# Kernel optimization log

Hardware: AMD Instinct MI355X
Metric: run time of the kernel (lower is better)

The kernel has to match this reference:

```python
import jax, jax.numpy as jnp
import numpy as np

N = 50000      # nodes
E = 800000     # edges (before self-loops)
H = 4          # heads
C = 64         # hidden channels per head
CLS = 10       # len(bins)+1
D_IN = 64      # input feature dim
NEG_SLOPE = 0.2


def setup_inputs() -> dict:
    key = jax.random.key(0)
    ks = jax.random.split(key, 24)
    inp = {
        "x": jax.random.normal(ks[0], (N, D_IN), jnp.float32),
        "edge_index": jax.random.randint(ks[1], (2, E), 0, N),
    }
    dims = [(D_IN, C), (H * C, C), (H * C, C), (H * C, C), (H * C, CLS)]
    k = 2
    for l, (din, dout) in enumerate(dims):
        sc = 1.0 / np.sqrt(din)
        inp[f"W{l}"] = jax.random.normal(ks[k], (din, H * dout), jnp.float32) * sc; k += 1
        inp[f"as{l}"] = jax.random.normal(ks[k], (H, dout), jnp.float32) * sc; k += 1
        inp[f"ad{l}"] = jax.random.normal(ks[k], (H, dout), jnp.float32) * sc; k += 1
        inp[f"b{l}"] = jnp.zeros((H * dout,), jnp.float32)
    return inp


def gat_layer(x, src, dst, W, a_s, a_d, b):
    # PyG GATConv (concat=True): h = x W -> [N,H,Ch]
    Hh, Ch = a_s.shape
    h = (x @ W).reshape(-1, Hh, Ch)
    asn = (h * a_s).sum(-1)                      # [N,H]
    adn = (h * a_d).sum(-1)                      # [N,H]
    e = jax.nn.leaky_relu(asn[src] + adn[dst], NEG_SLOPE)   # [Et,H]
    m = jax.ops.segment_max(e, dst, num_segments=N)         # softmax over in-edges per dst
    ex = jnp.exp(e - m[dst])
    s = jax.ops.segment_sum(ex, dst, num_segments=N)
    alpha = ex / (s[dst] + 1e-16)                # [Et,H]
    out = jax.ops.segment_sum(alpha[:, :, None] * h[src], dst, num_segments=N)
    return out.reshape(-1, Hh * Ch) + b


def reference(x, edge_index, W0, as0, ad0, b0, W1, as1, ad1, b1,
              W2, as2, ad2, b2, W3, as3, ad3, b3, W4, as4, ad4, b4):
    loop = jnp.arange(N, dtype=edge_index.dtype)  # GATConv add_self_loops=True
    src = jnp.concatenate([edge_index[0], loop])
    dst = jnp.concatenate([edge_index[1], loop])
    params = [(W0, as0, ad0, b0), (W1, as1, ad1, b1), (W2, as2, ad2, b2),
              (W3, as3, ad3, b3), (W4, as4, ad4, b4)]
    for W, a_s, a_d, b in params:
        x = jax.nn.relu(gat_layer(x, src, dst, W, a_s, a_d, b))
        # dropout(p=0.5) is identity in eval mode (training=False)
    return x
```

## Files before the change

### kernel.cpp

```cpp
#include <hip/hip_runtime.h>
#include <hip/hip_bf16.h>
#include <math.h>

#define N_NODES 50000
#define N_PAD   50048
#define N_EDGES 800000
#define HEADS 4

typedef __attribute__((ext_vector_type(8))) _Float16 half8_t;
typedef __attribute__((ext_vector_type(4))) float f32x4;

__device__ inline void split2(float v, _Float16& p0, _Float16& p1) {
    p0 = (_Float16)v;
    p1 = (_Float16)(v - (float)p0);
}


__global__ void init_deg_kernel(int* __restrict__ deg) {
    int i = blockIdx.x * blockDim.x + threadIdx.x;
    if (i < N_NODES) deg[i] = 1;
}

__global__ void hist_kernel(const int* __restrict__ dst, int* __restrict__ deg) {
    int i = blockIdx.x * blockDim.x + threadIdx.x;
    if (i < N_EDGES) atomicAdd(&deg[dst[i]], 1);
}

__global__ __launch_bounds__(1024) void scan_kernel(const int* __restrict__ deg,
                                                    int* __restrict__ rowptr,
                                                    int* __restrict__ cursor) {
    __shared__ int wsums[16];
    const int t = threadIdx.x;
    const int wv = t >> 6, ln = t & 63;
    const int WCHUNK = (N_NODES + 15) / 16;
    const int base = wv * WCHUNK;
    int lim = base + WCHUNK; if (lim > N_NODES) lim = N_NODES;

    int tot = 0;
    for (int i = base + ln; i < lim; i += 64) tot += deg[i];
#pragma unroll
    for (int o = 1; o < 64; o <<= 1) tot += __shfl_xor(tot, o);
    if (ln == 0) wsums[wv] = tot;
    __syncthreads();

    int run = 0;
    for (int w = 0; w < wv; ++w) run += wsums[w];

    for (int i0 = base; i0 < lim; i0 += 64) {
        int i = i0 + ln;
        int d = (i < lim) ? deg[i] : 0;
        int sc = d;
#pragma unroll
        for (int o = 1; o < 64; o <<= 1) {
            int v = __shfl_up(sc, o);
            if (ln >= o) sc += v;
        }
        if (i < lim) {
            int val = run + sc - d;
            rowptr[i] = val;
            cursor[i] = val;
        }
        run += __shfl(sc, 63);
    }
    if (t == 1023) rowptr[N_NODES] = run;
}

__global__ void scatter_kernel(const int* __restrict__ src, const int* __restrict__ dst,
                               int* __restrict__ cursor, int* __restrict__ col) {
    int i = blockIdx.x * blockDim.x + threadIdx.x;
    if (i < N_EDGES) {
        int d = dst[i];
        int pos = atomicAdd(&cursor[d], 1);
        col[pos] = src[i];
    } else if (i < N_EDGES + N_NODES) {
        int n = i - N_EDGES;
        int pos = atomicAdd(&cursor[n], 1);
        col[pos] = n;
    }
}


__global__ void x_split_kernel(const float* __restrict__ x, _Float16* __restrict__ pl,
                               size_t pstride) {
    int i = blockIdx.x * blockDim.x + threadIdx.x;
    if (i >= N_NODES * 64) return;
    _Float16 a, b;
    split2(x[i], a, b);
    pl[i] = a;
    pl[pstride + i] = b;
}

__global__ void w_split_kernel(const float* __restrict__ W, _Float16* __restrict__ wt,
                               int K, int NC) {
    int t = blockIdx.x * blockDim.x + threadIdx.x;
    int c = t >> 8, k = t & 255;
    float v = (k < K && c < NC) ? W[k * NC + c] : 0.f;
    _Float16 a, b;
    split2(v, a, b);
    wt[t] = a;
    wt[65536 + t] = b;
}


template <int FUSE_ATTN>
__global__ __launch_bounds__(256) void gemm_mfma_kernel(
        const _Float16* __restrict__ Apl, size_t apstride, int lda,
        const _Float16* __restrict__ Wt,
        float* __restrict__ C, int K, int NC,
        const float* __restrict__ as_flat, const float* __restrict__ ad_flat,
        float* __restrict__ asn, float* __restrict__ adn) {
    __shared__ _Float16 As[2][128][40];
    __shared__ _Float16 Bs[2][128][40];

    const int tid = threadIdx.x;
    const int lane = tid & 63;
    const int wave = tid >> 6;
    const int wr = (wave >> 1) * 64;
    const int wc = (wave & 1) * 64;
    const int m0 = blockIdx.x * 128;
    const int n0 = blockIdx.y * 128;

    f32x4 acc[4][4];
#pragma unroll
    for (int i = 0; i < 4; ++i)
#pragma unroll
        for (int j = 0; j < 4; ++j) acc[i][j] = (f32x4){0.f, 0.f, 0.f, 0.f};

    const int row0 = tid >> 2, q = tid & 3;
    const int row1 = row0 + 64;

    const _Float16* aptr0 = Apl + (size_t)(m0 + row0) * lda + q * 8;
    const _Float16* aptr1 = Apl + (size_t)(m0 + row1) * lda + q * 8;
    const _Float16* bptr0 = Wt + (size_t)(n0 + row0) * 256 + q * 8;
    const _Float16* bptr1 = Wt + (size_t)(n0 + row1) * 256 + q * 8;

    half8_t pa[2][2], pb[2][2];
#pragma unroll
    for (int p = 0; p < 2; ++p) {
        pa[p][0] = *(const half8_t*)(aptr0 + p * apstride);
        pa[p][1] = *(const half8_t*)(aptr1 + p * apstride);
        pb[p][0] = *(const half8_t*)(bptr0 + p * 65536);
        pb[p][1] = *(const half8_t*)(bptr1 + p * 65536);
    }

    for (int k0 = 0; k0 < K; k0 += 32) {
        if (k0) __syncthreads();
#pragma unroll
        for (int p = 0; p < 2; ++p) {
            *(half8_t*)(&As[p][row0][q * 8]) = pa[p][0];
            *(half8_t*)(&As[p][row1][q * 8]) = pa[p][1];
            *(half8_t*)(&Bs[p][row0][q * 8]) = pb[p][0];
            *(half8_t*)(&Bs[p][row1][q * 8]) = pb[p][1];
        }
        __syncthreads();

        if (k0 + 32 < K) {
            int kn = k0 + 32;
#pragma unroll
            for (int p = 0; p < 2; ++p) {
                pa[p][0] = *(const half8_t*)(aptr0 + p * apstride + kn);
                pa[p][1] = *(const half8_t*)(aptr1 + p * apstride + kn);
                pb[p][0] = *(const half8_t*)(bptr0 + p * 65536 + kn);
                pb[p][1] = *(const half8_t*)(bptr1 + p * 65536 + kn);
            }
        }

        half8_t bf[2][4];
#pragma unroll
        for (int p = 0; p < 2; ++p)
#pragma unroll
            for (int j = 0; j < 4; ++j)
                bf[p][j] = *(const half8_t*)(&Bs[p][wc + j * 16 + (lane & 15)][(lane >> 4) * 8]);

#pragma unroll
        for (int i = 0; i < 4; ++i) {
            half8_t af0 = *(const half8_t*)(&As[0][wr + i * 16 + (lane & 15)][(lane >> 4) * 8]);
            half8_t af1 = *(const half8_t*)(&As[1][wr + i * 16 + (lane & 15)][(lane >> 4) * 8]);
#pragma unroll
            for (int j = 0; j < 4; ++j) {
                f32x4 c = acc[i][j];
                c = __builtin_amdgcn_mfma_f32_16x16x32_f16(af0, bf[1][j], c, 0, 0, 0);
                c = __builtin_amdgcn_mfma_f32_16x16x32_f16(af1, bf[0][j], c, 0, 0, 0);
                c = __builtin_amdgcn_mfma_f32_16x16x32_f16(af0, bf[0][j], c, 0, 0, 0);
                acc[i][j] = c;
            }
        }
    }

    const int rbase = m0 + wr + (lane >> 4) * 4;
    const int cbase = n0 + wc + (lane & 15);
#pragma unroll
    for (int i = 0; i < 4; ++i)
#pragma unroll
        for (int j = 0; j < 4; ++j) {
            int gcol = cbase + j * 16;
            if (gcol >= NC) continue;
#pragma unroll
            for (int r4 = 0; r4 < 4; ++r4) {
                int grow = rbase + i * 16 + r4;
                if (grow < N_NODES) C[(size_t)grow * NC + gcol] = acc[i][j][r4];
            }
        }

    if (FUSE_ATTN) {
        const int hd_out = (n0 + wc) >> 6;
        float as_v[4], ad_v[4];
#pragma unroll
        for (int j = 0; j < 4; ++j) {
            int gc = cbase + j * 16;
            as_v[j] = as_flat[gc];
            ad_v[j] = ad_flat[gc];
        }
#pragma unroll
        for (int i = 0; i < 4; ++i)
#pragma unroll
            for (int r4 = 0; r4 < 4; ++r4) {
                float ps = 0.f, pd = 0.f;
#pragma unroll
                for (int j = 0; j < 4; ++j) {
                    float v = acc[i][j][r4];
                    ps += v * as_v[j];
                    pd += v * ad_v[j];
                }
#pragma unroll
                for (int o = 1; o < 16; o <<= 1) {
                    ps += __shfl_xor(ps, o);
                    pd += __shfl_xor(pd, o);
                }
                if ((lane & 15) == 0) {
                    int grow = rbase + i * 16 + r4;
                    if (grow < N_NODES) {
                        asn[grow * 4 + hd_out] = ps;
                        adn[grow * 4 + hd_out] = pd;
                    }
                }
            }
    }
}


__global__ void attn_coef_kernel(const float* __restrict__ h,
                                 const float* __restrict__ a_s,
                                 const float* __restrict__ a_d,
                                 float* __restrict__ asn, float* __restrict__ adn,
                                 int CH) {
    int t = blockIdx.x * blockDim.x + threadIdx.x;
    if (t >= N_NODES * HEADS) return;
    int n = t >> 2;
    int hd = t & 3;
    const float* hp = h + (size_t)n * HEADS * CH + hd * CH;
    const float* sp = a_s + hd * CH;
    const float* dp = a_d + hd * CH;
    float s1 = 0.f, s2 = 0.f;
    for (int c = 0; c < CH; c += 2) {
        float2 hv = *reinterpret_cast<const float2*>(&hp[c]);
        float2 av = *reinterpret_cast<const float2*>(&sp[c]);
        float2 dv = *reinterpret_cast<const float2*>(&dp[c]);
        s1 += hv.x * av.x + hv.y * av.y;
        s2 += hv.x * dv.x + hv.y * dv.y;
    }
    asn[t] = s1;
    adn[t] = s2;
}


template <int CH, int EMIT>
__global__ __launch_bounds__(256) void aggregate_kernel(
        const float* __restrict__ h, const float* __restrict__ asn,
        const float* __restrict__ adn, const int* __restrict__ rowptr,
        const int* __restrict__ col, const float* __restrict__ bias,
        _Float16* __restrict__ pl, size_t pstride, float* __restrict__ out) {
    constexpr int HC = HEADS * CH;
    __shared__ float2 pair_lds[HEADS][32];

    const int n = blockIdx.x;
    const int hd = threadIdx.x >> 6;
    const int lane = threadIdx.x & 63;
    const int el = lane & 31;
    const int hdoff = hd * CH + lane;

    const int start = rowptr[n];
    const int end = rowptr[n + 1];
    const float adv = adn[(n << 2) | hd];

    float m = -INFINITY, s = 0.f;
    float accv[4] = {0.f, 0.f, 0.f, 0.f};

    for (int e0 = start; e0 < end; e0 += 32) {
        int e = e0 + el;
        bool valid = (lane < 32) && (e < end);
        int srcl = n;
        float ev = -INFINITY;
        if (valid) {
            srcl = col[e];
            float t = asn[(srcl << 2) | hd] + adv;
            ev = (t > 0.f) ? t : 0.2f * t;
        }
        float bm = ev;
#pragma unroll
        for (int o = 1; o < 64; o <<= 1) bm = fmaxf(bm, __shfl_xor(bm, o));
        float mn = fmaxf(m, bm);
        float scale = __expf(m - mn);
        float p = __expf(ev - mn);
        float ps = p;
#pragma unroll
        for (int o = 1; o < 64; o <<= 1) ps += __shfl_xor(ps, o);
        s = s * scale + ps;
#pragma unroll
        for (int c = 0; c < 4; ++c) accv[c] *= scale;
        m = mn;

        if (lane < 32) pair_lds[hd][lane] = make_float2(__int_as_float(srcl), p);

        int cnt = end - e0; if (cnt > 32) cnt = 32;
        int cnt8 = (cnt + 7) & ~7;
        for (int i0 = 0; i0 < cnt8; i0 += 8) {
            int sv[8]; float pv[8];
#pragma unroll
            for (int j = 0; j < 8; ++j) {
                float2 pr = pair_lds[hd][i0 + j];
                sv[j] = __float_as_int(pr.x);
                pv[j] = pr.y;
            }
            float hv[8];
#pragma unroll
            for (int j = 0; j < 8; ++j)
                hv[j] = (lane < CH) ? h[(size_t)sv[j] * HC + hdoff] : 0.f;
#pragma unroll
            for (int j = 0; j < 8; ++j) accv[j & 3] += pv[j] * hv[j];
        }
    }

    if (lane < CH) {
        float acc = (accv[0] + accv[1]) + (accv[2] + accv[3]);
        float v = acc / (s + 1e-16f) + bias[hd * CH + lane];
        v = fmaxf(v, 0.f);
        if (EMIT) {
            _Float16 a, b;
            split2(v, a, b);
            size_t off = (size_t)n * HC + hd * CH + lane;
            pl[off] = a;
            pl[pstride + off] = b;
        } else {
            out[n * HC + hd * CH + lane] = v;
        }
    }
}


extern "C" void kernel_launch(void* const* d_in, const int* in_sizes, int n_in,
                              void* d_out, int out_size, void* d_ws, size_t ws_size,
                              hipStream_t stream) {
    const float* x_in = (const float*)d_in[0];
    const int* ei = (const int*)d_in[1];
    const int* src = ei;
    const int* dst = ei + N_EDGES;

    const float *W[5], *AS[5], *AD[5], *BI[5];
    for (int l = 0; l < 5; ++l) {
        W[l]  = (const float*)d_in[2 + l * 4 + 0];
        AS[l] = (const float*)d_in[2 + l * 4 + 1];
        AD[l] = (const float*)d_in[2 + l * 4 + 2];
        BI[l] = (const float*)d_in[2 + l * 4 + 3];
    }

    const size_t PSTRIDE = (size_t)N_PAD * 256;
    _Float16* planes = (_Float16*)d_ws;
    float* Hb   = (float*)(planes + 2 * PSTRIDE);
    float* asn  = Hb + (size_t)N_NODES * 256;
    float* adn  = asn + (size_t)N_NODES * HEADS;
    int* rowptr = (int*)(adn + (size_t)N_NODES * HEADS);
    int* cursor = rowptr + (N_NODES + 1);
    int* col    = cursor + N_NODES;
    _Float16* wt = (_Float16*)(((uintptr_t)(col + N_EDGES + N_NODES) + 15) & ~(uintptr_t)15);

    init_deg_kernel<<<(N_NODES + 255) / 256, 256, 0, stream>>>(cursor);
    hist_kernel<<<(N_EDGES + 255) / 256, 256, 0, stream>>>(dst, cursor);
    scan_kernel<<<1, 1024, 0, stream>>>(cursor, rowptr, cursor);
    scatter_kernel<<<(N_EDGES + N_NODES + 255) / 256, 256, 0, stream>>>(src, dst, cursor, col);

    for (int l = 0; l < 5; ++l) {
        int Kl = (l == 0) ? 64 : 256;
        int NCl = (l == 4) ? 40 : 256;
        w_split_kernel<<<256, 256, 0, stream>>>(W[l], wt + (size_t)l * 2 * 65536, Kl, NCl);
    }
    x_split_kernel<<<(N_NODES * 64 + 255) / 256, 256, 0, stream>>>(x_in, planes, PSTRIDE);

    int lda = 64;
    for (int l = 0; l < 5; ++l) {
        const int K = (l == 0) ? 64 : 256;
        const int NC = (l == 4) ? 40 : 256;
        dim3 ggrid(N_PAD / 128, (NC + 127) / 128);
        const _Float16* wl = wt + (size_t)l * 2 * 65536;
        if (l < 4) {
            gemm_mfma_kernel<1><<<ggrid, 256, 0, stream>>>(
                planes, PSTRIDE, lda, wl, Hb, K, NC, AS[l], AD[l], asn, adn);
            aggregate_kernel<64, 1><<<N_NODES, 256, 0, stream>>>(
                Hb, asn, adn, rowptr, col, BI[l], planes, PSTRIDE, nullptr);
        } else {
            gemm_mfma_kernel<0><<<ggrid, 256, 0, stream>>>(
                planes, PSTRIDE, lda, wl, Hb, K, NC, AS[l], AD[l], asn, adn);
            attn_coef_kernel<<<(N_NODES * HEADS + 255) / 256, 256, 0, stream>>>(
                Hb, AS[l], AD[l], asn, adn, 10);
            aggregate_kernel<10, 0><<<N_NODES, 256, 0, stream>>>(
                Hb, asn, adn, rowptr, col, BI[l], nullptr, 0, (float*)d_out);
        }
        lda = 256;
    }
    (void)in_sizes; (void)n_in; (void)out_size; (void)ws_size;
}
```

Before: 946.0 us.

## Store GEMM output as split fp16 planes and aggregate one node per wave

For the hidden layers the GEMM epilogue now writes h as two fp16 planes (hi and lo) instead of fp32. A new aggregation kernel handles one destination node per wave, with 16 lanes per head. It gathers neighbour rows as half4 vectors from both planes and uses an online softmax. The gather traffic per edge stays similar, but the layout and the finer per-wave granularity should cut latency and improve occupancy, at the cost of extra conversion arithmetic and a larger workspace.

```diff
diff --git a/kernel.cpp b/kernel.cpp
--- a/kernel.cpp
+++ b/kernel.cpp
@@ -8,6 +8,7 @@
 #define HEADS 4
 
 typedef __attribute__((ext_vector_type(8))) _Float16 half8_t;
+typedef __attribute__((ext_vector_type(4))) _Float16 half4_t;
 typedef __attribute__((ext_vector_type(4))) float f32x4;
 
 __device__ inline void split2(float v, _Float16& p0, _Float16& p1) {
@@ -106,6 +107,7 @@
 __global__ __launch_bounds__(256) void gemm_mfma_kernel(
         const _Float16* __restrict__ Apl, size_t apstride, int lda,
         const _Float16* __restrict__ Wt,
+        _Float16* __restrict__ hpl, size_t hstride,
         float* __restrict__ C, int K, int NC,
         const float* __restrict__ as_flat, const float* __restrict__ ad_flat,
         float* __restrict__ asn, float* __restrict__ adn) {
@@ -189,20 +191,25 @@
 
     const int rbase = m0 + wr + (lane >> 4) * 4;
     const int cbase = n0 + wc + (lane & 15);
-#pragma unroll
-    for (int i = 0; i < 4; ++i)
-#pragma unroll
-        for (int j = 0; j < 4; ++j) {
-            int gcol = cbase + j * 16;
-            if (gcol >= NC) continue;
-#pragma unroll
-            for (int r4 = 0; r4 < 4; ++r4) {
-                int grow = rbase + i * 16 + r4;
-                if (grow < N_NODES) C[(size_t)grow * NC + gcol] = acc[i][j][r4];
-            }
-        }
 
     if (FUSE_ATTN) {
+#pragma unroll
+        for (int i = 0; i < 4; ++i)
+#pragma unroll
+            for (int j = 0; j < 4; ++j) {
+                int gcol = cbase + j * 16;
+#pragma unroll
+                for (int r4 = 0; r4 < 4; ++r4) {
+                    int grow = rbase + i * 16 + r4;
+                    if (grow < N_NODES) {
+                        _Float16 a, b;
+                        split2(acc[i][j][r4], a, b);
+                        size_t off = (size_t)grow * 256 + gcol;
+                        hpl[off] = a;
+                        hpl[hstride + off] = b;
+                    }
+                }
+            }
         const int hd_out = (n0 + wc) >> 6;
         float as_v[4], ad_v[4];
 #pragma unroll
@@ -233,6 +240,19 @@
                         asn[grow * 4 + hd_out] = ps;
                         adn[grow * 4 + hd_out] = pd;
                     }
+                }
+            }
+    } else {
+#pragma unroll
+        for (int i = 0; i < 4; ++i)
+#pragma unroll
+            for (int j = 0; j < 4; ++j) {
+                int gcol = cbase + j * 16;
+                if (gcol >= NC) continue;
+#pragma unroll
+                for (int r4 = 0; r4 < 4; ++r4) {
+                    int grow = rbase + i * 16 + r4;
+                    if (grow < N_NODES) C[(size_t)grow * NC + gcol] = acc[i][j][r4];
                 }
             }
     }
@@ -264,12 +284,100 @@
 }
 
 
-template <int CH, int EMIT>
-__global__ __launch_bounds__(256) void aggregate_kernel(
+__global__ __launch_bounds__(256) void aggregate64_kernel(
+        const _Float16* __restrict__ hpl, size_t hstride,
+        const float* __restrict__ asn, const float* __restrict__ adn,
+        const int* __restrict__ rowptr, const int* __restrict__ col,
+        const float* __restrict__ bias,
+        _Float16* __restrict__ pl, size_t pstride) {
+    const int n = (blockIdx.x << 2) + (threadIdx.x >> 6);
+    const int lane = threadIdx.x & 63;
+    const int hd = lane >> 4;
+    const int e16 = lane & 15;
+    const int pbase = lane & 48;
+
+    const int start = rowptr[n];
+    const int end = rowptr[n + 1];
+    const float adv = adn[(n << 2) | hd];
+
+    float m = -INFINITY, s = 0.f;
+    float a0 = 0.f, a1 = 0.f, a2 = 0.f, a3 = 0.f;
+
+    for (int e0 = start; e0 < end; e0 += 16) {
+        int e = e0 + e16;
+        int srcl = n;
+        float ev = -INFINITY;
+        if (e < end) {
+            srcl = col[e];
+            float t = asn[(srcl << 2) | hd] + adv;
+            ev = (t > 0.f) ? t : 0.2f * t;
+        }
+        float bm = ev;
+#pragma unroll
+        for (int o = 1; o < 16; o <<= 1) bm = fmaxf(bm, __shfl_xor(bm, o));
+        float mn = fmaxf(m, bm);
+        float scale = __expf(m - mn);
+        float p = __expf(ev - mn);
+        float ps = p;
+#pragma unroll
+        for (int o = 1; o < 16; o <<= 1) ps += __shfl_xor(ps, o);
+        s = s * scale + ps;
+        a0 *= scale; a1 *= scale; a2 *= scale; a3 *= scale;
+        m = mn;
+
+        int cnt = end - e0; if (cnt > 16) cnt = 16;
+        int cnt4 = (cnt + 3) & ~3;
+        for (int j0 = 0; j0 < cnt4; j0 += 4) {
+            int sj[4]; float pj[4];
+#pragma unroll
+            for (int j = 0; j < 4; ++j) {
+                sj[j] = __shfl(srcl, j0 + j);
+                pj[j] = __shfl(p, pbase + j0 + j);
+            }
+            half4_t h0[4], h1[4];
+#pragma unroll
+            for (int j = 0; j < 4; ++j) {
+                const _Float16* hp = hpl + (size_t)sj[j] * 256 + (lane << 2);
+                h0[j] = *(const half4_t*)hp;
+                h1[j] = *(const half4_t*)(hp + hstride);
+            }
+#pragma unroll
+            for (int j = 0; j < 4; ++j) {
+                a0 += pj[j] * ((float)h0[j][0] + (float)h1[j][0]);
+                a1 += pj[j] * ((float)h0[j][1] + (float)h1[j][1]);
+                a2 += pj[j] * ((float)h0[j][2] + (float)h1[j][2]);
+                a3 += pj[j] * ((float)h0[j][3] + (float)h1[j][3]);
+            }
+        }
+    }
+
+    float sd = s + 1e-16f;
+    const float* bp = bias + (lane << 2);
+    float v0 = fmaxf(a0 / sd + bp[0], 0.f);
+    float v1 = fmaxf(a1 / sd + bp[1], 0.f);
+    float v2 = fmaxf(a2 / sd + bp[2], 0.f);
+    float v3 = fmaxf(a3 / sd + bp[3], 0.f);
+
+    _Float16 s0a, s0b, s1a, s1b, s2a, s2b, s3a, s3b;
+    split2(v0, s0a, s0b);
+    split2(v1, s1a, s1b);
+    split2(v2, s2a, s2b);
+    split2(v3, s3a, s3b);
+    half4_t o0, o1;
+    o0[0] = s0a; o0[1] = s1a; o0[2] = s2a; o0[3] = s3a;
+    o1[0] = s0b; o1[1] = s1b; o1[2] = s2b; o1[3] = s3b;
+    size_t off = (size_t)n * 256 + (lane << 2);
+    *(half4_t*)(pl + off) = o0;
+    *(half4_t*)(pl + pstride + off) = o1;
+}
+
+
+template <int CH>
+__global__ __launch_bounds__(256) void aggregate_out_kernel(
         const float* __restrict__ h, const float* __restrict__ asn,
         const float* __restrict__ adn, const int* __restrict__ rowptr,
         const int* __restrict__ col, const float* __restrict__ bias,
-        _Float16* __restrict__ pl, size_t pstride, float* __restrict__ out) {
+        float* __restrict__ out) {
     constexpr int HC = HEADS * CH;
     __shared__ float2 pair_lds[HEADS][32];
 
@@ -334,16 +442,7 @@
     if (lane < CH) {
         float acc = (accv[0] + accv[1]) + (accv[2] + accv[3]);
         float v = acc / (s + 1e-16f) + bias[hd * CH + lane];
-        v = fmaxf(v, 0.f);
-        if (EMIT) {
-            _Float16 a, b;
-            split2(v, a, b);
-            size_t off = (size_t)n * HC + hd * CH + lane;
-            pl[off] = a;
-            pl[pstride + off] = b;
-        } else {
-            out[n * HC + hd * CH + lane] = v;
-        }
+        out[n * HC + hd * CH + lane] = fmaxf(v, 0.f);
     }
 }
 
@@ -366,8 +465,9 @@
 
     const size_t PSTRIDE = (size_t)N_PAD * 256;
     _Float16* planes = (_Float16*)d_ws;
-    float* Hb   = (float*)(planes + 2 * PSTRIDE);
-    float* asn  = Hb + (size_t)N_NODES * 256;
+    _Float16* hpl = planes + 2 * PSTRIDE;
+    float* Hb   = (float*)(hpl + 2 * PSTRIDE);
+    float* asn  = Hb + (size_t)N_NODES * 40;
     float* adn  = asn + (size_t)N_NODES * HEADS;
     int* rowptr = (int*)(adn + (size_t)N_NODES * HEADS);
     int* cursor = rowptr + (N_NODES + 1);
@@ -394,16 +494,18 @@
         const _Float16* wl = wt + (size_t)l * 2 * 65536;
         if (l < 4) {
             gemm_mfma_kernel<1><<<ggrid, 256, 0, stream>>>(
-                planes, PSTRIDE, lda, wl, Hb, K, NC, AS[l], AD[l], asn, adn);
-            aggregate_kernel<64, 1><<<N_NODES, 256, 0, stream>>>(
-                Hb, asn, adn, rowptr, col, BI[l], planes, PSTRIDE, nullptr);
+                planes, PSTRIDE, lda, wl, hpl, PSTRIDE, nullptr, K, NC,
+                AS[l], AD[l], asn, adn);
+            aggregate64_kernel<<<N_NODES / 4, 256, 0, stream>>>(
+                hpl, PSTRIDE, asn, adn, rowptr, col, BI[l], planes, PSTRIDE);
         } else {
             gemm_mfma_kernel<0><<<ggrid, 256, 0, stream>>>(
-                planes, PSTRIDE, lda, wl, Hb, K, NC, AS[l], AD[l], asn, adn);
+                planes, PSTRIDE, lda, wl, nullptr, 0, Hb, K, NC,
+                AS[l], AD[l], asn, adn);
             attn_coef_kernel<<<(N_NODES * HEADS + 255) / 256, 256, 0, stream>>>(
                 Hb, AS[l], AD[l], asn, adn, 10);
-            aggregate_kernel<10, 0><<<N_NODES, 256, 0, stream>>>(
-                Hb, asn, adn, rowptr, col, BI[l], nullptr, 0, (float*)d_out);
+            aggregate_out_kernel<10><<<N_NODES, 256, 0, stream>>>(
+                Hb, asn, adn, rowptr, col, BI[l], (float*)d_out);
         }
         lda = 256;
     }
```

Result: no change. 933.3 us (-1.3%).
